# Kernel tuning notes

Hardware: AMD Instinct MI355X
Metric: run time of the kernel (lower is better)

## Reference

```python
import jax, jax.numpy as jnp
import numpy as np

TEMPERATURE = 0.07
KNN_AUG = True
NUM_NEIGHBORS = 10
B, N, D = 2048, 65536, 128
NUM_CLUSTERS = 100
EPS = 1e-12


def _l2_normalize(x):
    # matches torch F.normalize(dim=1): x / max(||x||, eps)
    norm = jnp.sqrt(jnp.sum(x * x, axis=1, keepdims=True))
    return x / jnp.maximum(norm, EPS)


def setup_inputs() -> dict:
    key = jax.random.key(0)
    k1, k2, k3, k4 = jax.random.split(key, 4)
    return {
        "features": jax.random.normal(k1, (B, D), dtype=jnp.float32),
        "cluster_idxes": jax.random.randint(k2, (B,), 0, NUM_CLUSTERS),
        "global_features": jax.random.normal(k3, (N, D), dtype=jnp.float32),
        "global_clusters": jax.random.randint(k4, (N,), 0, NUM_CLUSTERS),
    }


def reference(features, cluster_idxes, global_features, global_clusters):
    f = _l2_normalize(features)            # [B, D]
    g = _l2_normalize(global_features)     # [N, D]
    sim = (f @ g.T) / TEMPERATURE          # [B, N]

    # cluster-membership positive mask: [B, N]
    pos_mask = (cluster_idxes[:, None] == global_clusters[None, :]).astype(sim.dtype)

    if KNN_AUG:
        k_val = min(NUM_NEIGHBORS, sim.shape[-1])
        _, knn_idx = jax.lax.top_k(sim, k_val)  # [B, k]
        rows = jnp.arange(sim.shape[0])[:, None]
        knn_mask = jnp.zeros_like(pos_mask).at[rows, knn_idx].set(1.0)
        pos_mask = ((pos_mask + knn_mask) > 0).astype(sim.dtype)

    # masked log-softmax reduction (same math as original: exp/sum/log)
    log_prob = sim - jnp.log(jnp.sum(jnp.exp(sim), axis=1, keepdims=True) + EPS)  # [B, N]
    mean_log_prob_pos = jnp.sum(pos_mask * log_prob, axis=1) / (jnp.sum(pos_mask, axis=1) + EPS)
    return -jnp.mean(mean_log_prob_pos)
```

## Files before the change

kernel.cpp:

```cpp
#include <hip/hip_runtime.h>

#define B_ROWS 2048
#define N_GLB  65536
#define DDIM   128
#define NCLUST 100
#define INV_T  (1.0f/0.07f)
#define LOG2E  1.4426950408889634f
#define LN2    0.6931471805599453f
#define NSPLIT 16
#define CHUNK_COLS (N_GLB/NSPLIT)
#define ITERS (CHUNK_COLS/64)
#define ROWSB 32
#define GRPB 2048
#define TOPK 10
#define CAP  256
#define NSLICE 8
#define TAU_L2E (3.7881f*LOG2E)
#define CSC    65536.0f
#define INV_CSC (1.0f/65536.0f)

typedef __attribute__((ext_vector_type(4))) float f32x4;
typedef __attribute__((ext_vector_type(2))) long lg2;
typedef unsigned long long u64;

__device__ __forceinline__ unsigned fmono(float v) {
  unsigned u = __float_as_uint(v);
  return ((int)u < 0) ? ~u : (u | 0x80000000u);
}
__device__ __forceinline__ float fmono_inv(unsigned m) {
  unsigned u = (m & 0x80000000u) ? (m & 0x7FFFFFFFu) : ~m;
  return __uint_as_float(u);
}
__device__ __forceinline__ u64 mkkey(float val, int col) {
  return ((u64)fmono(val) << 32) | (unsigned)(~(unsigned)col);
}
__device__ __forceinline__ u64 umax64(u64 a, u64 b) { return a > b ? a : b; }

__device__ __forceinline__ float fp8d(unsigned b) {
  unsigned e = (b >> 3) & 15, m = b & 7;
  float v = e ? __uint_as_float(((e + 120u) << 23) | (m << 20))
              : (float)m * 0.001953125f;
  return (b & 0x80u) ? -v : v;
}

__global__ __launch_bounds__(256) void prep_kernel(
    const float* __restrict__ f, const float* __restrict__ g,
    char* __restrict__ wsf2, char* __restrict__ wsg2,
    float* __restrict__ inv_fT) {
  __shared__ unsigned short lds[1024];
  const int t = threadIdx.x, lane = t & 63, w = t >> 6;
  const int grp = blockIdx.x;
  const bool isf = grp < (B_ROWS / 16);

  #pragma unroll
  for (int j = 0; j < 4; ++j) {
    int rit = w * 4 + j;
    int row = grp * 16 + rit;
    int rr = isf ? row : row - B_ROWS;
    const float* src = (isf ? f : g) + (size_t)rr * DDIM;
    float2 v = ((const float2*)src)[lane];
    float ss = v.x * v.x + v.y * v.y;
    #pragma unroll
    for (int m = 32; m; m >>= 1) ss += __shfl_xor(ss, m);
    float inv = 1.0f / fmaxf(sqrtf(ss), 1e-12f);
    if (isf && lane == 0) inv_fT[rr] = inv * INV_T;
    float sc = isf ? inv * (INV_T * LOG2E) : inv;
    unsigned pk = __builtin_amdgcn_cvt_pk_fp8_f32(v.x * sc, v.y * sc, 0u, false);
    int k = 2 * lane;
    int off = ((k >> 6) << 10) + (((k >> 3) & 3) << 8) + (rit << 4)
            + (((k >> 5) & 1) << 3) + (k & 7);
    lds[off >> 1] = (unsigned short)(pk & 0xFFFFu);
  }
  __syncthreads();
  char* dst = isf ? (wsf2 + (size_t)grp * GRPB)
                  : (wsg2 + (size_t)(grp - B_ROWS / 16) * GRPB);
  if (t < 128) ((uint4*)dst)[t] = ((const uint4*)lds)[t];
}

__global__ __launch_bounds__(256) void csum2_kernel(
    const char* __restrict__ wsg2, const int* __restrict__ gclust,
    int* __restrict__ csum_i32, int* __restrict__ hist8) {
  __shared__ int cs[NCLUST * DDIM];
  __shared__ int hcnt[NCLUST];
  const int t = threadIdx.x, lane = t & 63, w = t >> 6;
  for (int i = t; i < NCLUST * DDIM; i += 256) cs[i] = 0;
  if (t < NCLUST) hcnt[t] = 0;
  __syncthreads();

  const int rbase = blockIdx.x * 512;
  const int rg = lane >> 4;
  const int ch = lane & 15;
  const int p = ch >> 1, h = ch & 1;
  const int kbase = ((p >> 2) << 6) + (h << 5) + ((p & 3) << 3);
  for (int step = 0; step < 32; ++step) {
    int row = rbase + step * 16 + w * 4 + rg;
    int c = gclust[row];
    uint2 v = *(const uint2*)(wsg2 + (size_t)(row >> 4) * GRPB + (p >> 2) * 1024
                              + (p & 3) * 256 + (row & 15) * 16 + h * 8);
    int* dst = &cs[c * DDIM + kbase];
    #pragma unroll
    for (int b = 0; b < 4; ++b) {
      atomicAdd(dst + b,     (int)rintf(fp8d((v.x >> (8 * b)) & 0xFFu) * CSC));
      atomicAdd(dst + 4 + b, (int)rintf(fp8d((v.y >> (8 * b)) & 0xFFu) * CSC));
    }
    if (ch == 0) atomicAdd(&hcnt[c], 1);
  }
  __syncthreads();
  const int slice = blockIdx.x & (NSLICE - 1);
  for (int i = t; i < NCLUST * DDIM; i += 256) {
    int x = cs[i];
    if (x) atomicAdd(&csum_i32[(size_t)slice * NCLUST * DDIM + i], x);
  }
  if (t < NCLUST && hcnt[t]) atomicAdd(&hist8[slice * 128 + t], hcnt[t]);
}

#define PUSHQ(av, mm, q)                                                        \
  if ((av) > TAU_L2E) {                                                         \
    int rw = r0 + (mm) * 16 + lhi * 4 + (q);                                    \
    int slot = atomicAdd(&cnt[rw], 1);                                          \
    if (slot < CAP) { lv[rw * CAP + slot] = (av) * LN2; li[rw * CAP + slot] = colv; } \
  }

#define EPI(a, mm)                                                              \
  {                                                                             \
    se[mm].x += __builtin_amdgcn_exp2f(a.x);                                    \
    se[mm].y += __builtin_amdgcn_exp2f(a.y);                                    \
    se[mm].z += __builtin_amdgcn_exp2f(a.z);                                    \
    se[mm].w += __builtin_amdgcn_exp2f(a.w);                                    \
    float mx = fmaxf(fmaxf(a.x, a.y), fmaxf(a.z, a.w));                         \
    if (mx > TAU_L2E) { PUSHQ(a.x, mm, 0) PUSHQ(a.y, mm, 1) PUSHQ(a.z, mm, 2) PUSHQ(a.w, mm, 3) } \
  }

#define LOADB(dst, gptr)                                                        \
  { dst[0] = *(const uint4*)((gptr) + (size_t)lane * 16);                       \
    dst[1] = *(const uint4*)((gptr) + 1024 + (size_t)lane * 16); }

#define COMPUTE_REFILL(bb, itv, refbase, dorefill)                              \
  {                                                                             \
    f32x4 ac0 = {0,0,0,0}, ac1 = {0,0,0,0};                                     \
    _Pragma("unroll") for (int sp = 0; sp < 2; ++sp) {                          \
      lg2 bsp = __builtin_bit_cast(lg2, bb[sp]);                                \
      if (dorefill)                                                             \
        bb[sp] = *(const uint4*)((refbase) + sp * 1024 + (size_t)lane * 16);    \
      ac0 = __builtin_amdgcn_mfma_f32_16x16x32_fp8_fp8(afr[0][sp][0], bsp[0], ac0, 0, 0, 0); \
      ac1 = __builtin_amdgcn_mfma_f32_16x16x32_fp8_fp8(afr[1][sp][0], bsp[0], ac1, 0, 0, 0); \
      ac0 = __builtin_amdgcn_mfma_f32_16x16x32_fp8_fp8(afr[0][sp][1], bsp[1], ac0, 0, 0, 0); \
      ac1 = __builtin_amdgcn_mfma_f32_16x16x32_fp8_fp8(afr[1][sp][1], bsp[1], ac1, 0, 0, 0); \
    }                                                                           \
    const int colv = chunk * CHUNK_COLS + (itv) * 64 + w * 16 + l15;            \
    EPI(ac0, 0) EPI(ac1, 1)                                                     \
  }

__global__ __launch_bounds__(256, 4) void sim_kernel(
    const char* __restrict__ wsf2, const char* __restrict__ wsg2,
    float* __restrict__ p_se, float* __restrict__ lv, int* __restrict__ li,
    int* __restrict__ cnt) {
  __shared__ float sered[4][ROWSB];
  const int t = threadIdx.x, lane = t & 63, w = t >> 6;
  const int l15 = lane & 15, lhi = lane >> 4;
  const int chunk = blockIdx.x;
  const int r0 = blockIdx.y * ROWSB;

  const char* fbase = wsf2 + (size_t)(r0 >> 4) * GRPB;
  lg2 afr[2][2];
  #pragma unroll
  for (int m = 0; m < 2; ++m)
    #pragma unroll
    for (int sp = 0; sp < 2; ++sp)
      afr[m][sp] = __builtin_bit_cast(lg2,
        *(const uint4*)(fbase + (size_t)m * GRPB + sp * 1024 + (size_t)lane * 16));

  f32x4 z = {0.f, 0.f, 0.f, 0.f};
  f32x4 se[2] = {z, z};

  const char* gb = wsg2 + (size_t)(chunk * (CHUNK_COLS / 16) + w) * GRPB;
  uint4 b0[2], b1[2], b2[2], b3[2];
  LOADB(b0, gb)
  LOADB(b1, gb + 1 * 8192)
  LOADB(b2, gb + 2 * 8192)
  LOADB(b3, gb + 3 * 8192)
  for (int it = 0; it < ITERS; it += 4) {
    COMPUTE_REFILL(b0, it,     gb + 4 * 8192, it + 4 < ITERS)
    COMPUTE_REFILL(b1, it + 1, gb + 5 * 8192, it + 5 < ITERS)
    COMPUTE_REFILL(b2, it + 2, gb + 6 * 8192, it + 6 < ITERS)
    COMPUTE_REFILL(b3, it + 3, gb + 7 * 8192, it + 7 < ITERS)
    gb += 4 * 8192;
  }

  #pragma unroll
  for (int m = 0; m < 2; ++m)
    #pragma unroll
    for (int q = 0; q < 4; ++q) {
      float s = se[m][q];
      s += __shfl_xor(s, 1); s += __shfl_xor(s, 2);
      s += __shfl_xor(s, 4); s += __shfl_xor(s, 8);
      if (l15 == 0) sered[w][m * 16 + lhi * 4 + q] = s;
    }
  __syncthreads();
  if (t < ROWSB) {
    float s = sered[0][t] + sered[1][t] + sered[2][t] + sered[3][t];
    p_se[(size_t)(r0 + t) * NSPLIT + chunk] = s;
  }
}

__global__ __launch_bounds__(256) void merge_kernel(
    const float* __restrict__ f, const int* __restrict__ fclust,
    const int* __restrict__ gclust, const float* __restrict__ inv_fT,
    const float* __restrict__ p_se, const int* __restrict__ csum_i32,
    const int* __restrict__ hist8, const float* __restrict__ lv,
    const int* __restrict__ li, const int* __restrict__ cnt,
    const char* __restrict__ wsf2, const char* __restrict__ wsg2,
    float* __restrict__ rowv) {
  const int lane = threadIdx.x & 63, w = threadIdx.x >> 6;
  const int r = blockIdx.x * 4 + w;

  float sev = (lane < NSPLIT) ? p_se[(size_t)r * NSPLIT + lane] : 0.f;
  sev += __shfl_xor(sev, 8); sev += __shfl_xor(sev, 4);
  sev += __shfl_xor(sev, 2); sev += __shfl_xor(sev, 1);
  sev = __shfl(sev, 0);

  int rc = fclust[r];
  float2 fv = ((const float2*)(f + (size_t)r * DDIM))[lane];
  float sc = inv_fT[r];
  int ia = 0, ib = 0, hc = 0;
  #pragma unroll
  for (int s = 0; s < NSLICE; ++s) {
    ia += csum_i32[(size_t)s * NCLUST * DDIM + rc * DDIM + 2 * lane];
    ib += csum_i32[(size_t)s * NCLUST * DDIM + rc * DDIM + 2 * lane + 1];
    hc += hist8[s * 128 + rc];
  }
  float dt = fv.x * sc * (ia * INV_CSC) + fv.y * sc * (ib * INV_CSC);
  #pragma unroll
  for (int m = 32; m; m >>= 1) dt += __shfl_xor(dt, m);
  dt = __shfl(dt, 0);

  float Cc = (float)hc;
  int n = cnt[r];
  bool bad = (n < TOPK) || (n > CAP);
  float S10 = 0.f, C10 = 0.f;
  if (!bad) {
    u64 k0 = 0, k1 = 0, k2 = 0, k3 = 0;
    int e = lane;
    if (e < n) k0 = mkkey(lv[(size_t)r * CAP + e], li[(size_t)r * CAP + e]);
    e = lane + 64;
    if (e < n) k1 = mkkey(lv[(size_t)r * CAP + e], li[(size_t)r * CAP + e]);
    e = lane + 128;
    if (e < n) k2 = mkkey(lv[(size_t)r * CAP + e], li[(size_t)r * CAP + e]);
    e = lane + 192;
    if (e < n) k3 = mkkey(lv[(size_t)r * CAP + e], li[(size_t)r * CAP + e]);
    for (int it = 0; it < TOPK; ++it) {
      u64 best = umax64(umax64(k0, k1), umax64(k2, k3));
      #pragma unroll
      for (int m = 32; m; m >>= 1) best = umax64(best, __shfl_xor(best, m));
      float val = fmono_inv((unsigned)(best >> 32));
      int col = (int)(~(unsigned)(best & 0xFFFFFFFFull));
      int gc = gclust[col];
      if (gc != rc) { S10 += val; C10 += 1.f; }
      if (k0 == best) k0 = 0;
      if (k1 == best) k1 = 0;
      if (k2 == best) k2 = 0;
      if (k3 == best) k3 = 0;
    }
  } else {
    uint4 fr[8];
    #pragma unroll
    for (int pc = 0; pc < 8; ++pc)
      fr[pc] = *(const uint4*)(wsf2 + (size_t)(r >> 4) * GRPB + (pc >> 2) * 1024
                               + (pc & 3) * 256 + (r & 15) * 16);
    u64 tk[TOPK];
    #pragma unroll
    for (int i = 0; i < TOPK; ++i) tk[i] = 0;
    for (int col = lane; col < N_GLB; col += 64) {
      const char* gp = wsg2 + (size_t)(col >> 4) * GRPB + (col & 15) * 16;
      float acc = 0.f;
      #pragma unroll
      for (int pc = 0; pc < 8; ++pc) {
        uint4 gv = *(const uint4*)(gp + (pc >> 2) * 1024 + (pc & 3) * 256);
        uint4 fc = fr[pc];
        #pragma unroll
        for (int wd = 0; wd < 4; ++wd) {
          unsigned fa = (&fc.x)[wd], ga = (&gv.x)[wd];
          #pragma unroll
          for (int b = 0; b < 4; ++b)
            acc += fp8d((fa >> (8 * b)) & 0xFFu) * fp8d((ga >> (8 * b)) & 0xFFu);
        }
      }
      u64 key = mkkey(acc, col);
      if (key > tk[0]) {
        u64 cur = key;
        #pragma unroll
        for (int i = 0; i < TOPK - 1; ++i) {
          u64 nxt = tk[i + 1];
          u64 lo = cur < nxt ? cur : nxt;
          u64 hi = cur < nxt ? nxt : cur;
          tk[i] = lo; cur = hi;
        }
        tk[TOPK - 1] = cur;
      }
    }
    for (int it = 0; it < TOPK; ++it) {
      u64 best = tk[TOPK - 1];
      #pragma unroll
      for (int m = 32; m; m >>= 1) best = umax64(best, __shfl_xor(best, m));
      float val = fmono_inv((unsigned)(best >> 32)) * LN2;
      int col = (int)(~(unsigned)(best & 0xFFFFFFFFull));
      if (gclust[col] != rc) { S10 += val; C10 += 1.f; }
      if (tk[TOPK - 1] == best) {
        #pragma unroll
        for (int i = TOPK - 1; i > 0; --i) tk[i] = tk[i - 1];
        tk[0] = 0;
      }
    }
  }
  if (lane == 0) {
    float L = logf(sev + 1e-12f);
    float C = Cc + C10;
    rowv[r] = (dt + S10 - C * L) / (C + 1e-12f);
  }
}

__global__ void final_kernel(const float* __restrict__ rowv, float* __restrict__ out) {
  __shared__ float sm[256];
  int t = threadIdx.x;
  float s = 0.f;
  for (int i = t; i < B_ROWS; i += 256) s += rowv[i];
  sm[t] = s;
  __syncthreads();
  for (int o = 128; o; o >>= 1) { if (t < o) sm[t] += sm[t + o]; __syncthreads(); }
  if (t == 0) out[0] = -(sm[0] / (float)B_ROWS);
}

extern "C" void kernel_launch(void* const* d_in, const int* in_sizes, int n_in,
                              void* d_out, int out_size, void* d_ws, size_t ws_size,
                              hipStream_t stream) {
  const float* f  = (const float*)d_in[0];
  const int*   fc = (const int*)  d_in[1];
  const float* g  = (const float*)d_in[2];
  const int*   gc = (const int*)  d_in[3];
  float* out = (float*)d_out;

  char* ws = (char*)d_ws;
  char*  wsf2    = ws;
  char*  wsg2    = ws + 262144;
  float* inv_fT  = (float*)(ws + 8650752);
  float* p_se    = (float*)(ws + 8658944);
  int*   csum_i32= (int*)  (ws + 8790016);
  int*   hist8   = (int*)  (ws + 9199616);
  int*   cnt     = (int*)  (ws + 9203712);
  float* lv      = (float*)(ws + 9211904);
  int*   li      = (int*)  (ws + 11309056);
  float* rowv    = (float*)(ws + 13406208);

  hipMemsetAsync(ws + 8790016, 0, 421888, stream);

  prep_kernel<<<(B_ROWS + N_GLB) / 16, 256, 0, stream>>>(f, g, wsf2, wsg2, inv_fT);

  csum2_kernel<<<N_GLB / 512, 256, 0, stream>>>(wsg2, gc, csum_i32, hist8);

  dim3 grid(NSPLIT, B_ROWS / ROWSB);
  sim_kernel<<<grid, 256, 0, stream>>>(wsf2, wsg2, p_se, lv, li, cnt);

  merge_kernel<<<B_ROWS / 4, 256, 0, stream>>>(f, fc, gc, inv_fT, p_se, csum_i32,
                                               hist8, lv, li, cnt, wsf2, wsg2, rowv);
  final_kernel<<<1, 256, 0, stream>>>(rowv, out);
}
```

Before: 124.8 us.

## Halve sim row tile, raise occupancy, and build cluster sums from fp32

The sim kernel now processes 16 feature rows per block instead of 32. It splits the K reduction across two accumulators, uses a shallower two-stage prefetch of B tiles, and raises launch bounds to 8 blocks per SM, aiming for more parallelism and lower register pressure. The cluster-sum kernel now reads the original fp32 global features scaled by a stored inverse norm instead of decoding fp8, which changes precision and adds global-memory reads. The smaller row tile doubles reads of the global matrix across blocks.

```diff
diff --git a/kernel.cpp b/kernel.cpp
--- a/kernel.cpp
+++ b/kernel.cpp
@@ -10,7 +10,7 @@
 #define NSPLIT 16
 #define CHUNK_COLS (N_GLB/NSPLIT)
 #define ITERS (CHUNK_COLS/64)
-#define ROWSB 32
+#define ROWSB 16
 #define GRPB 2048
 #define TOPK 10
 #define CAP  256
@@ -46,7 +46,7 @@
 __global__ __launch_bounds__(256) void prep_kernel(
     const float* __restrict__ f, const float* __restrict__ g,
     char* __restrict__ wsf2, char* __restrict__ wsg2,
-    float* __restrict__ inv_fT) {
+    float* __restrict__ inv_fT, float* __restrict__ inv_g) {
   __shared__ unsigned short lds[1024];
   const int t = threadIdx.x, lane = t & 63, w = t >> 6;
   const int grp = blockIdx.x;
@@ -63,7 +63,7 @@
     #pragma unroll
     for (int m = 32; m; m >>= 1) ss += __shfl_xor(ss, m);
     float inv = 1.0f / fmaxf(sqrtf(ss), 1e-12f);
-    if (isf && lane == 0) inv_fT[rr] = inv * INV_T;
+    if (lane == 0) { if (isf) inv_fT[rr] = inv * INV_T; else inv_g[rr] = inv; }
     float sc = isf ? inv * (INV_T * LOG2E) : inv;
     unsigned pk = __builtin_amdgcn_cvt_pk_fp8_f32(v.x * sc, v.y * sc, 0u, false);
     int k = 2 * lane;
@@ -78,7 +78,8 @@
 }
 
 __global__ __launch_bounds__(256) void csum2_kernel(
-    const char* __restrict__ wsg2, const int* __restrict__ gclust,
+    const float* __restrict__ g, const int* __restrict__ gclust,
+    const float* __restrict__ inv_g,
     int* __restrict__ csum_i32, int* __restrict__ hist8) {
   __shared__ int cs[NCLUST * DDIM];
   __shared__ int hcnt[NCLUST];
@@ -90,19 +91,22 @@
   const int rbase = blockIdx.x * 512;
   const int rg = lane >> 4;
   const int ch = lane & 15;
-  const int p = ch >> 1, h = ch & 1;
-  const int kbase = ((p >> 2) << 6) + (h << 5) + ((p & 3) << 3);
   for (int step = 0; step < 32; ++step) {
     int row = rbase + step * 16 + w * 4 + rg;
     int c = gclust[row];
-    uint2 v = *(const uint2*)(wsg2 + (size_t)(row >> 4) * GRPB + (p >> 2) * 1024
-                              + (p & 3) * 256 + (row & 15) * 16 + h * 8);
-    int* dst = &cs[c * DDIM + kbase];
-    #pragma unroll
-    for (int b = 0; b < 4; ++b) {
-      atomicAdd(dst + b,     (int)rintf(fp8d((v.x >> (8 * b)) & 0xFFu) * CSC));
-      atomicAdd(dst + 4 + b, (int)rintf(fp8d((v.y >> (8 * b)) & 0xFFu) * CSC));
-    }
+    float scale = inv_g[row] * CSC;
+    const float* gp = g + (size_t)row * DDIM + 8 * ch;
+    float4 a = *(const float4*)gp;
+    float4 b = *(const float4*)(gp + 4);
+    int* dst = &cs[c * DDIM + ch * 8];
+    atomicAdd(dst + 0, (int)rintf(a.x * scale));
+    atomicAdd(dst + 1, (int)rintf(a.y * scale));
+    atomicAdd(dst + 2, (int)rintf(a.z * scale));
+    atomicAdd(dst + 3, (int)rintf(a.w * scale));
+    atomicAdd(dst + 4, (int)rintf(b.x * scale));
+    atomicAdd(dst + 5, (int)rintf(b.y * scale));
+    atomicAdd(dst + 6, (int)rintf(b.z * scale));
+    atomicAdd(dst + 7, (int)rintf(b.w * scale));
     if (ch == 0) atomicAdd(&hcnt[c], 1);
   }
   __syncthreads();
@@ -114,21 +118,11 @@
   if (t < NCLUST && hcnt[t]) atomicAdd(&hist8[slice * 128 + t], hcnt[t]);
 }
 
-#define PUSHQ(av, mm, q)                                                        \
+#define PUSHQ(av, q)                                                            \
   if ((av) > TAU_L2E) {                                                         \
-    int rw = r0 + (mm) * 16 + lhi * 4 + (q);                                    \
+    int rw = r0 + lhi * 4 + (q);                                                \
     int slot = atomicAdd(&cnt[rw], 1);                                          \
     if (slot < CAP) { lv[rw * CAP + slot] = (av) * LN2; li[rw * CAP + slot] = colv; } \
-  }
-
-#define EPI(a, mm)                                                              \
-  {                                                                             \
-    se[mm].x += __builtin_amdgcn_exp2f(a.x);                                    \
-    se[mm].y += __builtin_amdgcn_exp2f(a.y);                                    \
-    se[mm].z += __builtin_amdgcn_exp2f(a.z);                                    \
-    se[mm].w += __builtin_amdgcn_exp2f(a.w);                                    \
-    float mx = fmaxf(fmaxf(a.x, a.y), fmaxf(a.z, a.w));                         \
-    if (mx > TAU_L2E) { PUSHQ(a.x, mm, 0) PUSHQ(a.y, mm, 1) PUSHQ(a.z, mm, 2) PUSHQ(a.w, mm, 3) } \
   }
 
 #define LOADB(dst, gptr)                                                        \
@@ -137,21 +131,30 @@
 
 #define COMPUTE_REFILL(bb, itv, refbase, dorefill)                              \
   {                                                                             \
-    f32x4 ac0 = {0,0,0,0}, ac1 = {0,0,0,0};                                     \
-    _Pragma("unroll") for (int sp = 0; sp < 2; ++sp) {                          \
-      lg2 bsp = __builtin_bit_cast(lg2, bb[sp]);                                \
-      if (dorefill)                                                             \
-        bb[sp] = *(const uint4*)((refbase) + sp * 1024 + (size_t)lane * 16);    \
-      ac0 = __builtin_amdgcn_mfma_f32_16x16x32_fp8_fp8(afr[0][sp][0], bsp[0], ac0, 0, 0, 0); \
-      ac1 = __builtin_amdgcn_mfma_f32_16x16x32_fp8_fp8(afr[1][sp][0], bsp[0], ac1, 0, 0, 0); \
-      ac0 = __builtin_amdgcn_mfma_f32_16x16x32_fp8_fp8(afr[0][sp][1], bsp[1], ac0, 0, 0, 0); \
-      ac1 = __builtin_amdgcn_mfma_f32_16x16x32_fp8_fp8(afr[1][sp][1], bsp[1], ac1, 0, 0, 0); \
+    f32x4 acA = {0,0,0,0}, acB = {0,0,0,0};                                     \
+    lg2 bs0 = __builtin_bit_cast(lg2, bb[0]);                                   \
+    lg2 bs1 = __builtin_bit_cast(lg2, bb[1]);                                   \
+    if (dorefill) {                                                             \
+      bb[0] = *(const uint4*)((refbase) + (size_t)lane * 16);                   \
+      bb[1] = *(const uint4*)((refbase) + 1024 + (size_t)lane * 16);            \
     }                                                                           \
-    const int colv = chunk * CHUNK_COLS + (itv) * 64 + w * 16 + l15;            \
-    EPI(ac0, 0) EPI(ac1, 1)                                                     \
-  }
-
-__global__ __launch_bounds__(256, 4) void sim_kernel(
+    acA = __builtin_amdgcn_mfma_f32_16x16x32_fp8_fp8(afr[0][0], bs0[0], acA, 0, 0, 0); \
+    acB = __builtin_amdgcn_mfma_f32_16x16x32_fp8_fp8(afr[1][0], bs1[0], acB, 0, 0, 0); \
+    acA = __builtin_amdgcn_mfma_f32_16x16x32_fp8_fp8(afr[0][1], bs0[1], acA, 0, 0, 0); \
+    acB = __builtin_amdgcn_mfma_f32_16x16x32_fp8_fp8(afr[1][1], bs1[1], acB, 0, 0, 0); \
+    f32x4 a = acA + acB;                                                        \
+    se.x += __builtin_amdgcn_exp2f(a.x);                                        \
+    se.y += __builtin_amdgcn_exp2f(a.y);                                        \
+    se.z += __builtin_amdgcn_exp2f(a.z);                                        \
+    se.w += __builtin_amdgcn_exp2f(a.w);                                        \
+    float mx = fmaxf(fmaxf(a.x, a.y), fmaxf(a.z, a.w));                         \
+    if (mx > TAU_L2E) {                                                         \
+      const int colv = chunk * CHUNK_COLS + (itv) * 64 + w * 16 + l15;          \
+      PUSHQ(a.x, 0) PUSHQ(a.y, 1) PUSHQ(a.z, 2) PUSHQ(a.w, 3)                   \
+    }                                                                           \
+  }
+
+__global__ __launch_bounds__(256, 8) void sim_kernel(
     const char* __restrict__ wsf2, const char* __restrict__ wsg2,
     float* __restrict__ p_se, float* __restrict__ lv, int* __restrict__ li,
     int* __restrict__ cnt) {
@@ -162,40 +165,31 @@
   const int r0 = blockIdx.y * ROWSB;
 
   const char* fbase = wsf2 + (size_t)(r0 >> 4) * GRPB;
-  lg2 afr[2][2];
-  #pragma unroll
-  for (int m = 0; m < 2; ++m)
-    #pragma unroll
-    for (int sp = 0; sp < 2; ++sp)
-      afr[m][sp] = __builtin_bit_cast(lg2,
-        *(const uint4*)(fbase + (size_t)m * GRPB + sp * 1024 + (size_t)lane * 16));
-
-  f32x4 z = {0.f, 0.f, 0.f, 0.f};
-  f32x4 se[2] = {z, z};
+  lg2 afr[2];
+  #pragma unroll
+  for (int sp = 0; sp < 2; ++sp)
+    afr[sp] = __builtin_bit_cast(lg2,
+      *(const uint4*)(fbase + sp * 1024 + (size_t)lane * 16));
+
+  f32x4 se = {0.f, 0.f, 0.f, 0.f};
 
   const char* gb = wsg2 + (size_t)(chunk * (CHUNK_COLS / 16) + w) * GRPB;
-  uint4 b0[2], b1[2], b2[2], b3[2];
+  uint4 b0[2], b1[2];
   LOADB(b0, gb)
-  LOADB(b1, gb + 1 * 8192)
-  LOADB(b2, gb + 2 * 8192)
-  LOADB(b3, gb + 3 * 8192)
-  for (int it = 0; it < ITERS; it += 4) {
-    COMPUTE_REFILL(b0, it,     gb + 4 * 8192, it + 4 < ITERS)
-    COMPUTE_REFILL(b1, it + 1, gb + 5 * 8192, it + 5 < ITERS)
-    COMPUTE_REFILL(b2, it + 2, gb + 6 * 8192, it + 6 < ITERS)
-    COMPUTE_REFILL(b3, it + 3, gb + 7 * 8192, it + 7 < ITERS)
-    gb += 4 * 8192;
-  }
-
-  #pragma unroll
-  for (int m = 0; m < 2; ++m)
-    #pragma unroll
-    for (int q = 0; q < 4; ++q) {
-      float s = se[m][q];
-      s += __shfl_xor(s, 1); s += __shfl_xor(s, 2);
-      s += __shfl_xor(s, 4); s += __shfl_xor(s, 8);
-      if (l15 == 0) sered[w][m * 16 + lhi * 4 + q] = s;
-    }
+  LOADB(b1, gb + 8192)
+  for (int it = 0; it < ITERS; it += 2) {
+    COMPUTE_REFILL(b0, it,     gb + 2 * 8192, it + 2 < ITERS)
+    COMPUTE_REFILL(b1, it + 1, gb + 3 * 8192, it + 3 < ITERS)
+    gb += 2 * 8192;
+  }
+
+  #pragma unroll
+  for (int q = 0; q < 4; ++q) {
+    float s = se[q];
+    s += __shfl_xor(s, 1); s += __shfl_xor(s, 2);
+    s += __shfl_xor(s, 4); s += __shfl_xor(s, 8);
+    if (l15 == 0) sered[w][lhi * 4 + q] = s;
+  }
   __syncthreads();
   if (t < ROWSB) {
     float s = sered[0][t] + sered[1][t] + sered[2][t] + sered[3][t];
@@ -343,19 +337,21 @@
   char*  wsf2    = ws;
   char*  wsg2    = ws + 262144;
   float* inv_fT  = (float*)(ws + 8650752);
-  float* p_se    = (float*)(ws + 8658944);
-  int*   csum_i32= (int*)  (ws + 8790016);
-  int*   hist8   = (int*)  (ws + 9199616);
-  int*   cnt     = (int*)  (ws + 9203712);
-  float* lv      = (float*)(ws + 9211904);
-  int*   li      = (int*)  (ws + 11309056);
-  float* rowv    = (float*)(ws + 13406208);
-
-  hipMemsetAsync(ws + 8790016, 0, 421888, stream);
-
-  prep_kernel<<<(B_ROWS + N_GLB) / 16, 256, 0, stream>>>(f, g, wsf2, wsg2, inv_fT);
-
-  csum2_kernel<<<N_GLB / 512, 256, 0, stream>>>(wsg2, gc, csum_i32, hist8);
+  float* inv_g   = (float*)(ws + 8658944);
+  float* p_se    = (float*)(ws + 8921088);
+  int*   csum_i32= (int*)  (ws + 9052160);
+  int*   hist8   = (int*)  (ws + 9461760);
+  int*   cnt     = (int*)  (ws + 9465856);
+  float* lv      = (float*)(ws + 9474048);
+  int*   li      = (int*)  (ws + 11571200);
+  float* rowv    = (float*)(ws + 13668352);
+
+  hipMemsetAsync(ws + 9052160, 0, 421888, stream);
+
+  prep_kernel<<<(B_ROWS + N_GLB) / 16, 256, 0, stream>>>(f, g, wsf2, wsg2,
+                                                         inv_fT, inv_g);
+
+  csum2_kernel<<<N_GLB / 512, 256, 0, stream>>>(g, gc, inv_g, csum_i32, hist8);
 
   dim3 grid(NSPLIT, B_ROWS / ROWSB);
   sim_kernel<<<grid, 256, 0, stream>>>(wsf2, wsg2, p_se, lv, li, cnt);
```

After: 116.3 us. -6.8%, faster.
